# Kernel tuning notes

Hardware: AMD Instinct MI355X
Metric: run time of the kernel (lower is better)

The kernel has to match this reference:

```python
import jax, jax.numpy as jnp
import numpy as np

B, N, F_IN, F_OUT, T, E = 2, 50000, 2, 32, 12, 800000


def _uniform(k, shape, scale):
    return jax.random.uniform(k, shape, jnp.float32, -scale, scale)


def setup_inputs() -> dict:
    key = jax.random.key(0)
    ks = jax.random.split(key, 18)
    inp = {
        "X": jax.random.normal(ks[0], (B, N, F_IN, T), dtype=jnp.float32),
        "edge_index": jax.random.randint(ks[1], (2, E), 0, N, dtype=jnp.int64),
        "edge_weight": jax.random.uniform(ks[2], (E,), dtype=jnp.float32),
    }
    # GCNConv weights [F_IN, F_OUT] (glorot) + bias, for gates z, r, h
    g = float(np.sqrt(6.0 / (F_IN + F_OUT)))
    inp["Wz"] = _uniform(ks[3], (F_IN, F_OUT), g); inp["bz"] = jnp.zeros((F_OUT,), jnp.float32)
    inp["Wr"] = _uniform(ks[4], (F_IN, F_OUT), g); inp["br"] = jnp.zeros((F_OUT,), jnp.float32)
    inp["Wh"] = _uniform(ks[5], (F_IN, F_OUT), g); inp["bh"] = jnp.zeros((F_OUT,), jnp.float32)
    # Linear(2*F_OUT -> F_OUT) per gate (stored as [2*F_OUT, F_OUT] for x @ W)
    l = float(np.sqrt(1.0 / (2 * F_OUT)))
    inp["Lz_w"] = _uniform(ks[6], (2 * F_OUT, F_OUT), l); inp["Lz_b"] = _uniform(ks[7], (F_OUT,), l)
    inp["Lr_w"] = _uniform(ks[8], (2 * F_OUT, F_OUT), l); inp["Lr_b"] = _uniform(ks[9], (F_OUT,), l)
    inp["Lh_w"] = _uniform(ks[10], (2 * F_OUT, F_OUT), l); inp["Lh_b"] = _uniform(ks[11], (F_OUT,), l)
    # attention logits over periods, init uniform(0,1)
    inp["attention"] = jax.random.uniform(ks[12], (T,), dtype=jnp.float32)
    return inp


def _a3tgcn(X, edge_index, edge_weight, Wz, bz, Wr, br, Wh, bh,
            Lz_w, Lz_b, Lr_w, Lr_b, Lh_w, Lh_b, attention):
    n = X.shape[1]
    loop = jnp.arange(n)
    row = jnp.concatenate([edge_index[0], loop])  # sources (+ self loops)
    col = jnp.concatenate([edge_index[1], loop])  # targets
    w = jnp.concatenate([edge_weight, jnp.ones((n,), X.dtype)])
    deg = jax.ops.segment_sum(w, col, num_segments=n)
    dinv = jnp.where(deg > 0, jax.lax.rsqrt(deg), 0.0)
    norm = dinv[row] * w * dinv[col]  # [E+N] sym-normalized coeffs

    def gcn(x, W, b):
        xw = jnp.einsum('bnf,fo->bno', x, W)                # [B,N,O]
        msg = xw[:, row, :] * norm[None, :, None]           # [B,E+N,O]
        agg = jax.vmap(lambda m: jax.ops.segment_sum(m, col, num_segments=n))(msg)
        return agg + b

    probs = jax.nn.softmax(attention)
    H0 = jnp.zeros((X.shape[0], n, Wz.shape[1]), X.dtype)

    def step(carry, inputs):
        H, acc = carry
        Xt, p = inputs  # Xt: [B,N,F_IN]
        Z = jax.nn.sigmoid(jnp.concatenate([gcn(Xt, Wz, bz), H], -1) @ Lz_w + Lz_b)
        R = jax.nn.sigmoid(jnp.concatenate([gcn(Xt, Wr, br), H], -1) @ Lr_w + Lr_b)
        Ht = jnp.tanh(jnp.concatenate([gcn(Xt, Wh, bh), H * R], -1) @ Lh_w + Lh_b)
        Hn = Z * H + (1.0 - Z) * Ht
        return (Hn, acc + p * Hn), None

    xs = jnp.moveaxis(X, -1, 0)  # [T,B,N,F_IN]
    (_, H_accum), _ = jax.lax.scan(step, (H0, H0), (xs, probs))
    return H_accum


def reference(X, edge_index, edge_weight, Wz, bz, Wr, br, Wh, bh,
              Lz_w, Lz_b, Lr_w, Lr_b, Lh_w, Lh_b, attention):
    return _a3tgcn(X, edge_index, edge_weight, Wz, bz, Wr, br, Wh, bh,
                   Lz_w, Lz_b, Lr_w, Lr_b, Lh_w, Lh_b, attention)
```

## Files before the change

kernel.cpp:

```cpp
#include <hip/hip_runtime.h>

#define NN 50000
#define EE 800000
#define TT 12
#define BB 2

#define OFF_AX   50048
#define OFF_P    2450048
#define OFF_CNT  2454144
#define OFF_OFF  2504192
#define OFF_CUR  2554240
#define OFF_BSUM 2604288
#define NB_SCAN  98
#define NNODES   (BB * NN)
#define NW       4
#define NBLK_REC 12500

__device__ __forceinline__ float fsig(float x) {
    x = fminf(fmaxf(x, -30.f), 30.f);
    return __builtin_amdgcn_rcpf(1.f + __expf(-x));
}
__device__ __forceinline__ float ftanh(float x) {
    x = fminf(fmaxf(x, -15.f), 15.f);
    float e = __expf(-2.f * x);
    return (1.f - e) * __builtin_amdgcn_rcpf(1.f + e);
}

__global__ void k_count(const int* __restrict__ idx, int* __restrict__ cnt) {
    int e = blockIdx.x * 256 + threadIdx.x;
    if (e < EE) atomicAdd(&cnt[idx[EE + e]], 1);
}

__global__ void k_scanA(const int* __restrict__ cnt, int* __restrict__ off,
                        int* __restrict__ bsum) {
    __shared__ int sm[512];
    int i = blockIdx.x * 512 + threadIdx.x;
    int v = (i < NN) ? cnt[i] : 0;
    sm[threadIdx.x] = v;
    __syncthreads();
#pragma unroll
    for (int d = 1; d < 512; d <<= 1) {
        int t = (threadIdx.x >= d) ? sm[threadIdx.x - d] : 0;
        __syncthreads();
        sm[threadIdx.x] += t;
        __syncthreads();
    }
    if (i < NN) off[i] = sm[threadIdx.x] - v;
    if (threadIdx.x == 511) bsum[blockIdx.x] = sm[511];
}

__global__ void k_scanB(int* __restrict__ bsum) {
    __shared__ int sm[128];
    int tid = threadIdx.x;
    int v = (tid < NB_SCAN) ? bsum[tid] : 0;
    sm[tid] = v;
    __syncthreads();
#pragma unroll
    for (int d = 1; d < 128; d <<= 1) {
        int t = (tid >= d) ? sm[tid - d] : 0;
        __syncthreads();
        sm[tid] += t;
        __syncthreads();
    }
    if (tid < NB_SCAN) bsum[tid] = sm[tid] - v;
}

__global__ void k_scanC(int* __restrict__ off, const int* __restrict__ bsum,
                        int* __restrict__ cur) {
    int i = blockIdx.x * 256 + threadIdx.x;
    if (i < NN) {
        int o = off[i] + bsum[i >> 9];
        off[i] = o;
        cur[i] = o;
    }
}

__global__ void k_fill(const int* __restrict__ idx, const float* __restrict__ w,
                       int* __restrict__ cur, int2* __restrict__ epack) {
    int e = blockIdx.x * 256 + threadIdx.x;
    if (e >= EE) return;
    int c = idx[EE + e];
    int s = atomicAdd(&cur[c], 1);
    epack[s] = make_int2(idx[e], __float_as_int(w[e]));
}

__global__ void k_degdinv(const int* __restrict__ off, const int* __restrict__ cnt,
                          const int2* __restrict__ epack, float* __restrict__ dinv) {
    int n = blockIdx.x * 256 + threadIdx.x;
    if (n >= NN) return;
    int s0 = off[n], c = cnt[n];
    float d = 1.f;
    for (int q = 0; q < c; q++) d += __int_as_float(epack[s0 + q].y);
    dinv[n] = rsqrtf(d);
}

__global__ __launch_bounds__(64) void k_gather(const float* __restrict__ X,
                                               const float* __restrict__ dinv,
                                               const int2* __restrict__ epack,
                                               const int* __restrict__ off,
                                               const int* __restrict__ cnt,
                                               float* __restrict__ AX) {
    int tid = blockIdx.x * 64 + threadIdx.x;
    if (tid >= NNODES) return;
    int b = tid / NN;
    int n = tid - b * NN;
    float di = dinv[n];
    const float* Xb = X + (size_t)b * NN * 24;

    float xf[24], acc[24];
    {
        const float4* xs = (const float4*)(Xb + (size_t)n * 24);
        float s = di * di;
#pragma unroll
        for (int q = 0; q < 6; q++) {
            float4 v = xs[q];
            xf[4 * q] = v.x; xf[4 * q + 1] = v.y; xf[4 * q + 2] = v.z; xf[4 * q + 3] = v.w;
        }
#pragma unroll
        for (int t = 0; t < TT; t++) {
            acc[2 * t] = s * xf[t];
            acc[2 * t + 1] = s * xf[12 + t];
        }
    }
    int s0 = off[n], c = cnt[n];
    for (int q = 0; q < c; q++) {
        int2 ep = epack[s0 + q];
        int r = ep.x;
        float nrm = dinv[r] * __int_as_float(ep.y) * di;
        const float4* xr = (const float4*)(Xb + (size_t)r * 24);
#pragma unroll
        for (int p = 0; p < 6; p++) {
            float4 v = xr[p];
            xf[4 * p] = v.x; xf[4 * p + 1] = v.y; xf[4 * p + 2] = v.z; xf[4 * p + 3] = v.w;
        }
#pragma unroll
        for (int t = 0; t < TT; t++) {
            acc[2 * t] = fmaf(nrm, xf[t], acc[2 * t]);
            acc[2 * t + 1] = fmaf(nrm, xf[12 + t], acc[2 * t + 1]);
        }
    }
    float4* o = (float4*)(AX + (size_t)tid * 24);
#pragma unroll
    for (int q = 0; q < 6; q++)
        o[q] = make_float4(acc[4 * q], acc[4 * q + 1], acc[4 * q + 2], acc[4 * q + 3]);
}

__global__ void k_fold(const float* __restrict__ Wz, const float* __restrict__ bz,
                       const float* __restrict__ Lwz, const float* __restrict__ Lbz,
                       const float* __restrict__ Wr, const float* __restrict__ br,
                       const float* __restrict__ Lwr, const float* __restrict__ Lbr,
                       const float* __restrict__ Wh, const float* __restrict__ bh,
                       const float* __restrict__ Lwh, const float* __restrict__ Lbh,
                       const float* __restrict__ att, float* __restrict__ P) {
    int tid = threadIdx.x;
    if (tid < 96) {
        int g = tid >> 5, j = tid & 31;
        const float* W  = g == 0 ? Wz  : (g == 1 ? Wr  : Wh);
        const float* b  = g == 0 ? bz  : (g == 1 ? br  : bh);
        const float* Lw = g == 0 ? Lwz : (g == 1 ? Lwr : Lwh);
        const float* Lb = g == 0 ? Lbz : (g == 1 ? Lbr : Lbh);
        float* out = P + g * 1120;
        float w0 = 0.f, w1 = 0.f, c = 0.f;
        for (int k = 0; k < 32; k++) {
            float lw = Lw[k * 32 + j];
            w0 += W[k] * lw;
            w1 += W[32 + k] * lw;
            c  += b[k] * lw;
        }
        out[j] = w0;
        out[32 + j] = w1;
        out[64 + j] = c + Lb[j];
        for (int k = 0; k < 32; k++) out[96 + k * 32 + j] = Lw[(32 + k) * 32 + j];
    } else if (tid == 96) {
        float m = -1e30f;
        for (int t = 0; t < TT; t++) m = fmaxf(m, att[t]);
        float s = 0.f;
        float e[TT];
        for (int t = 0; t < TT; t++) { e[t] = __expf(att[t] - m); s += e[t]; }
        for (int t = 0; t < TT; t++) P[3360 + t] = e[t] / s;
    }
}

__global__ __launch_bounds__(256) void k_recur(const float* __restrict__ AX,
                                               const float* __restrict__ P,
                                               float* __restrict__ out) {
    __shared__ __align__(16) float Hs[NW][32];
    __shared__ __align__(16) float rHs[NW][32];
    __shared__ __align__(16) float AXs[NW][24];
    const int lane = threadIdx.x & 63;
    const int w = threadIdx.x >> 6;
    const int j = lane & 31;
    const int h = lane >> 5;
    const int k0 = h * 16;
    const int gwave = blockIdx.x * NW + w;

    float LBz[16], LBr[16], LBh[16];
    float wz0 = P[j],        wz1 = P[32 + j],        cz = P[64 + j];
    float wr0 = P[1120 + j], wr1 = P[1120 + 32 + j], cr = P[1120 + 64 + j];
    float wh0 = P[2240 + j], wh1 = P[2240 + 32 + j], ch = P[2240 + 64 + j];
#pragma unroll
    for (int k = 0; k < 16; k++) {
        LBz[k] = P[96 + (k0 + k) * 32 + j];
        LBr[k] = P[1120 + 96 + (k0 + k) * 32 + j];
        LBh[k] = P[2240 + 96 + (k0 + k) * 32 + j];
    }

#pragma unroll 1
    for (int node = gwave; node < NNODES; node += NBLK_REC * NW) {
        if (lane < 24) AXs[w][lane] = AX[(size_t)node * 24 + lane];

        float2 a = *(const float2*)&AXs[w][0];
        float z = fsig(fmaf(a.x, wz0, fmaf(a.y, wz1, cz)));
        float th = ftanh(fmaf(a.x, wh0, fmaf(a.y, wh1, ch)));
        float H = (1.f - z) * th;
        float acc = P[3360] * H;
        if (lane < 32) Hs[w][j] = H;

#pragma unroll 1
        for (int t = 1; t < TT; t++) {
            a = *(const float2*)&AXs[w][2 * t];
            float hb[16];
#pragma unroll
            for (int i = 0; i < 4; i++) {
                float4 v = *(const float4*)&Hs[w][k0 + 4 * i];
                hb[4 * i] = v.x; hb[4 * i + 1] = v.y;
                hb[4 * i + 2] = v.z; hb[4 * i + 3] = v.w;
            }
            float sr;
            {
                float s0 = 0.f, s1 = 0.f, s2 = 0.f, s3 = 0.f;
#pragma unroll
                for (int k = 0; k < 16; k += 4) {
                    s0 = fmaf(hb[k],     LBr[k],     s0);
                    s1 = fmaf(hb[k + 1], LBr[k + 1], s1);
                    s2 = fmaf(hb[k + 2], LBr[k + 2], s2);
                    s3 = fmaf(hb[k + 3], LBr[k + 3], s3);
                }
                sr = (s0 + s1) + (s2 + s3);
            }
            sr += __shfl_xor(sr, 32, 64);
            float rH = fsig(fmaf(a.x, wr0, fmaf(a.y, wr1, cr)) + sr) * H;
            if (lane < 32) rHs[w][j] = rH;
            float sz;
            {
                float s0 = 0.f, s1 = 0.f, s2 = 0.f, s3 = 0.f;
#pragma unroll
                for (int k = 0; k < 16; k += 4) {
                    s0 = fmaf(hb[k],     LBz[k],     s0);
                    s1 = fmaf(hb[k + 1], LBz[k + 1], s1);
                    s2 = fmaf(hb[k + 2], LBz[k + 2], s2);
                    s3 = fmaf(hb[k + 3], LBz[k + 3], s3);
                }
                sz = (s0 + s1) + (s2 + s3);
            }
            sz += __shfl_xor(sz, 32, 64);
            z = fsig(fmaf(a.x, wz0, fmaf(a.y, wz1, cz)) + sz);
            float rb[16];
#pragma unroll
            for (int i = 0; i < 4; i++) {
                float4 v = *(const float4*)&rHs[w][k0 + 4 * i];
                rb[4 * i] = v.x; rb[4 * i + 1] = v.y;
                rb[4 * i + 2] = v.z; rb[4 * i + 3] = v.w;
            }
            float sh;
            {
                float s0 = 0.f, s1 = 0.f, s2 = 0.f, s3 = 0.f;
#pragma unroll
                for (int k = 0; k < 16; k += 4) {
                    s0 = fmaf(rb[k],     LBh[k],     s0);
                    s1 = fmaf(rb[k + 1], LBh[k + 1], s1);
                    s2 = fmaf(rb[k + 2], LBh[k + 2], s2);
                    s3 = fmaf(rb[k + 3], LBh[k + 3], s3);
                }
                sh = (s0 + s1) + (s2 + s3);
            }
            sh += __shfl_xor(sh, 32, 64);
            th = ftanh(fmaf(a.x, wh0, fmaf(a.y, wh1, ch)) + sh);
            float Hn = fmaf(z, H - th, th);
            H = Hn;
            acc = fmaf(P[3360 + t], Hn, acc);
            if (lane < 32 && t < TT - 1) Hs[w][j] = Hn;
        }
        if (lane < 32) out[(size_t)node * 32 + j] = acc;
    }
}

extern "C" void kernel_launch(void* const* d_in, const int* in_sizes, int n_in,
                              void* d_out, int out_size, void* d_ws, size_t ws_size,
                              hipStream_t stream) {
    const float* X   = (const float*)d_in[0];
    const int*   idx = (const int*)d_in[1];
    const float* ew  = (const float*)d_in[2];
    const float* Wz  = (const float*)d_in[3];
    const float* bz  = (const float*)d_in[4];
    const float* Wr  = (const float*)d_in[5];
    const float* br  = (const float*)d_in[6];
    const float* Wh  = (const float*)d_in[7];
    const float* bh  = (const float*)d_in[8];
    const float* Lwz = (const float*)d_in[9];
    const float* Lbz = (const float*)d_in[10];
    const float* Lwr = (const float*)d_in[11];
    const float* Lbr = (const float*)d_in[12];
    const float* Lwh = (const float*)d_in[13];
    const float* Lbh = (const float*)d_in[14];
    const float* att = (const float*)d_in[15];

    float* ws   = (float*)d_ws;
    float* dinv = ws;
    float* AX   = ws + OFF_AX;
    float* P    = ws + OFF_P;
    int*   cnt  = (int*)ws + OFF_CNT;
    int*   off  = (int*)ws + OFF_OFF;
    int*   cur  = (int*)ws + OFF_CUR;
    int*   bsum = (int*)ws + OFF_BSUM;
    float* out  = (float*)d_out;
    int2*  epack = (int2*)d_out;

    hipMemsetAsync(cnt, 0, NN * sizeof(int), stream);
    hipLaunchKernelGGL(k_count, dim3((EE + 255) / 256), dim3(256), 0, stream, idx, cnt);
    hipLaunchKernelGGL(k_scanA, dim3(NB_SCAN), dim3(512), 0, stream, cnt, off, bsum);
    hipLaunchKernelGGL(k_scanB, dim3(1), dim3(128), 0, stream, bsum);
    hipLaunchKernelGGL(k_scanC, dim3((NN + 255) / 256), dim3(256), 0, stream, off, bsum, cur);
    hipLaunchKernelGGL(k_fill, dim3((EE + 255) / 256), dim3(256), 0, stream, idx, ew, cur, epack);
    hipLaunchKernelGGL(k_degdinv, dim3((NN + 255) / 256), dim3(256), 0, stream, off, cnt, epack, dinv);
    hipLaunchKernelGGL(k_gather, dim3((NNODES + 63) / 64), dim3(64), 0, stream,
                       X, dinv, epack, off, cnt, AX);
    hipLaunchKernelGGL(k_fold, dim3(1), dim3(128), 0, stream,
                       Wz, bz, Lwz, Lbz, Wr, br, Lwr, Lbr, Wh, bh, Lwh, Lbh, att, P);
    hipLaunchKernelGGL(k_recur, dim3(NBLK_REC), dim3(256), 0, stream, AX, P, out);
}
```

Measured before the change: 319.4 us.

## Process two nodes per wave in GRU recurrence to interleave independent chains

Each wave now computes the 12-step gated recurrence for two nodes simultaneously, with duplicated shared-memory H/rH buffers and interleaved FMA chains. This exposes instruction-level parallelism across the serial per-step dependency chain and amortizes the register-resident weight loads over two nodes. The grid-stride loop is removed in favor of one pair per wave. Higher register use may reduce occupancy, partially bounded by a launch_bounds hint.

```diff
diff --git a/kernel.cpp b/kernel.cpp
--- a/kernel.cpp
+++ b/kernel.cpp
@@ -181,18 +181,19 @@
     }
 }
 
-__global__ __launch_bounds__(256) void k_recur(const float* __restrict__ AX,
-                                               const float* __restrict__ P,
-                                               float* __restrict__ out) {
-    __shared__ __align__(16) float Hs[NW][32];
-    __shared__ __align__(16) float rHs[NW][32];
-    __shared__ __align__(16) float AXs[NW][24];
+__global__ __launch_bounds__(256, 2) void k_recur(const float* __restrict__ AX,
+                                                  const float* __restrict__ P,
+                                                  float* __restrict__ out) {
+    __shared__ __align__(16) float Hs[NW][2][32];
+    __shared__ __align__(16) float rHs[NW][2][32];
+    __shared__ __align__(16) float AXs[NW][48];
     const int lane = threadIdx.x & 63;
     const int w = threadIdx.x >> 6;
     const int j = lane & 31;
     const int h = lane >> 5;
     const int k0 = h * 16;
-    const int gwave = blockIdx.x * NW + w;
+    const int pair = blockIdx.x * NW + w;
+    if (pair >= NNODES / 2) return;
 
     float LBz[16], LBr[16], LBh[16];
     float wz0 = P[j],        wz1 = P[32 + j],        cz = P[64 + j];
@@ -205,83 +206,98 @@
         LBh[k] = P[2240 + 96 + (k0 + k) * 32 + j];
     }
 
+    if (lane < 48) AXs[w][lane] = AX[(size_t)pair * 48 + lane];
+
+    float2 aA = *(const float2*)&AXs[w][0];
+    float2 aB = *(const float2*)&AXs[w][24];
+    float zA = fsig(fmaf(aA.x, wz0, fmaf(aA.y, wz1, cz)));
+    float zB = fsig(fmaf(aB.x, wz0, fmaf(aB.y, wz1, cz)));
+    float thA = ftanh(fmaf(aA.x, wh0, fmaf(aA.y, wh1, ch)));
+    float thB = ftanh(fmaf(aB.x, wh0, fmaf(aB.y, wh1, ch)));
+    float HA = (1.f - zA) * thA;
+    float HB = (1.f - zB) * thB;
+    float p0 = P[3360];
+    float accA = p0 * HA, accB = p0 * HB;
+    if (lane < 32) { Hs[w][0][j] = HA; Hs[w][1][j] = HB; }
+
 #pragma unroll 1
-    for (int node = gwave; node < NNODES; node += NBLK_REC * NW) {
-        if (lane < 24) AXs[w][lane] = AX[(size_t)node * 24 + lane];
-
-        float2 a = *(const float2*)&AXs[w][0];
-        float z = fsig(fmaf(a.x, wz0, fmaf(a.y, wz1, cz)));
-        float th = ftanh(fmaf(a.x, wh0, fmaf(a.y, wh1, ch)));
-        float H = (1.f - z) * th;
-        float acc = P[3360] * H;
-        if (lane < 32) Hs[w][j] = H;
-
-#pragma unroll 1
-        for (int t = 1; t < TT; t++) {
-            a = *(const float2*)&AXs[w][2 * t];
-            float hb[16];
+    for (int t = 1; t < TT; t++) {
+        aA = *(const float2*)&AXs[w][2 * t];
+        aB = *(const float2*)&AXs[w][24 + 2 * t];
+        float hbA[16], hbB[16];
+#pragma unroll
+        for (int i = 0; i < 4; i++) {
+            float4 vA = *(const float4*)&Hs[w][0][k0 + 4 * i];
+            float4 vB = *(const float4*)&Hs[w][1][k0 + 4 * i];
+            hbA[4 * i] = vA.x; hbA[4 * i + 1] = vA.y; hbA[4 * i + 2] = vA.z; hbA[4 * i + 3] = vA.w;
+            hbB[4 * i] = vB.x; hbB[4 * i + 1] = vB.y; hbB[4 * i + 2] = vB.z; hbB[4 * i + 3] = vB.w;
+        }
+        float srA, srB;
+        {
+            float a0 = 0.f, a1 = 0.f, b0 = 0.f, b1 = 0.f;
+#pragma unroll
+            for (int k = 0; k < 16; k += 2) {
+                a0 = fmaf(hbA[k],     LBr[k],     a0);
+                b0 = fmaf(hbB[k],     LBr[k],     b0);
+                a1 = fmaf(hbA[k + 1], LBr[k + 1], a1);
+                b1 = fmaf(hbB[k + 1], LBr[k + 1], b1);
+            }
+            srA = a0 + a1; srB = b0 + b1;
+        }
+        srA += __shfl_xor(srA, 32, 64);
+        srB += __shfl_xor(srB, 32, 64);
+        float rHA = fsig(fmaf(aA.x, wr0, fmaf(aA.y, wr1, cr)) + srA) * HA;
+        float rHB = fsig(fmaf(aB.x, wr0, fmaf(aB.y, wr1, cr)) + srB) * HB;
+        if (lane < 32) { rHs[w][0][j] = rHA; rHs[w][1][j] = rHB; }
+        float szA, szB;
+        {
+            float a0 = 0.f, a1 = 0.f, b0 = 0.f, b1 = 0.f;
+#pragma unroll
+            for (int k = 0; k < 16; k += 2) {
+                a0 = fmaf(hbA[k],     LBz[k],     a0);
+                b0 = fmaf(hbB[k],     LBz[k],     b0);
+                a1 = fmaf(hbA[k + 1], LBz[k + 1], a1);
+                b1 = fmaf(hbB[k + 1], LBz[k + 1], b1);
+            }
+            szA = a0 + a1; szB = b0 + b1;
+        }
+        szA += __shfl_xor(szA, 32, 64);
+        szB += __shfl_xor(szB, 32, 64);
+        zA = fsig(fmaf(aA.x, wz0, fmaf(aA.y, wz1, cz)) + szA);
+        zB = fsig(fmaf(aB.x, wz0, fmaf(aB.y, wz1, cz)) + szB);
+        float shA, shB;
+        {
+            float a0 = 0.f, a1 = 0.f, b0 = 0.f, b1 = 0.f;
 #pragma unroll
             for (int i = 0; i < 4; i++) {
-                float4 v = *(const float4*)&Hs[w][k0 + 4 * i];
-                hb[4 * i] = v.x; hb[4 * i + 1] = v.y;
-                hb[4 * i + 2] = v.z; hb[4 * i + 3] = v.w;
+                float4 vA = *(const float4*)&rHs[w][0][k0 + 4 * i];
+                float4 vB = *(const float4*)&rHs[w][1][k0 + 4 * i];
+                a0 = fmaf(vA.x, LBh[4 * i],     a0);
+                b0 = fmaf(vB.x, LBh[4 * i],     b0);
+                a1 = fmaf(vA.y, LBh[4 * i + 1], a1);
+                b1 = fmaf(vB.y, LBh[4 * i + 1], b1);
+                a0 = fmaf(vA.z, LBh[4 * i + 2], a0);
+                b0 = fmaf(vB.z, LBh[4 * i + 2], b0);
+                a1 = fmaf(vA.w, LBh[4 * i + 3], a1);
+                b1 = fmaf(vB.w, LBh[4 * i + 3], b1);
             }
-            float sr;
-            {
-                float s0 = 0.f, s1 = 0.f, s2 = 0.f, s3 = 0.f;
-#pragma unroll
-                for (int k = 0; k < 16; k += 4) {
-                    s0 = fmaf(hb[k],     LBr[k],     s0);
-                    s1 = fmaf(hb[k + 1], LBr[k + 1], s1);
-                    s2 = fmaf(hb[k + 2], LBr[k + 2], s2);
-                    s3 = fmaf(hb[k + 3], LBr[k + 3], s3);
-                }
-                sr = (s0 + s1) + (s2 + s3);
-            }
-            sr += __shfl_xor(sr, 32, 64);
-            float rH = fsig(fmaf(a.x, wr0, fmaf(a.y, wr1, cr)) + sr) * H;
-            if (lane < 32) rHs[w][j] = rH;
-            float sz;
-            {
-                float s0 = 0.f, s1 = 0.f, s2 = 0.f, s3 = 0.f;
-#pragma unroll
-                for (int k = 0; k < 16; k += 4) {
-                    s0 = fmaf(hb[k],     LBz[k],     s0);
-                    s1 = fmaf(hb[k + 1], LBz[k + 1], s1);
-                    s2 = fmaf(hb[k + 2], LBz[k + 2], s2);
-                    s3 = fmaf(hb[k + 3], LBz[k + 3], s3);
-                }
-                sz = (s0 + s1) + (s2 + s3);
-            }
-            sz += __shfl_xor(sz, 32, 64);
-            z = fsig(fmaf(a.x, wz0, fmaf(a.y, wz1, cz)) + sz);
-            float rb[16];
-#pragma unroll
-            for (int i = 0; i < 4; i++) {
-                float4 v = *(const float4*)&rHs[w][k0 + 4 * i];
-                rb[4 * i] = v.x; rb[4 * i + 1] = v.y;
-                rb[4 * i + 2] = v.z; rb[4 * i + 3] = v.w;
-            }
-            float sh;
-            {
-                float s0 = 0.f, s1 = 0.f, s2 = 0.f, s3 = 0.f;
-#pragma unroll
-                for (int k = 0; k < 16; k += 4) {
-                    s0 = fmaf(rb[k],     LBh[k],     s0);
-                    s1 = fmaf(rb[k + 1], LBh[k + 1], s1);
-                    s2 = fmaf(rb[k + 2], LBh[k + 2], s2);
-                    s3 = fmaf(rb[k + 3], LBh[k + 3], s3);
-                }
-                sh = (s0 + s1) + (s2 + s3);
-            }
-            sh += __shfl_xor(sh, 32, 64);
-            th = ftanh(fmaf(a.x, wh0, fmaf(a.y, wh1, ch)) + sh);
-            float Hn = fmaf(z, H - th, th);
-            H = Hn;
-            acc = fmaf(P[3360 + t], Hn, acc);
-            if (lane < 32 && t < TT - 1) Hs[w][j] = Hn;
-        }
-        if (lane < 32) out[(size_t)node * 32 + j] = acc;
+            shA = a0 + a1; shB = b0 + b1;
+        }
+        shA += __shfl_xor(shA, 32, 64);
+        shB += __shfl_xor(shB, 32, 64);
+        thA = ftanh(fmaf(aA.x, wh0, fmaf(aA.y, wh1, ch)) + shA);
+        thB = ftanh(fmaf(aB.x, wh0, fmaf(aB.y, wh1, ch)) + shB);
+        float HnA = fmaf(zA, HA - thA, thA);
+        float HnB = fmaf(zB, HB - thB, thB);
+        HA = HnA; HB = HnB;
+        float pt = P[3360 + t];
+        accA = fmaf(pt, HnA, accA);
+        accB = fmaf(pt, HnB, accB);
+        if (lane < 32 && t < TT - 1) { Hs[w][0][j] = HnA; Hs[w][1][j] = HnB; }
+    }
+    if (lane < 32) {
+        out[(size_t)pair * 64 + j] = accA;
+        out[(size_t)pair * 64 + 32 + j] = accB;
     }
 }
 
```

Measured after the change: 315.1 us, median of 2. About the same (-1.3%).
